# Performance work log

Measured on AMD Instinct MI355X. Metric: run time of the kernel, lower is better.

Reference implementation:

```python
import jax, jax.numpy as jnp
import numpy as np
import math

PERIODS = [4, 2, 1]          # period_num[-3:] sorted desc
SEQ, PRED, CH = 192, 96, 8
TOPM, DM = 20, 512
N_TRAIN, BSZ = 10000, 32


def decompose_mg(data):
    # data: [N, L, C] -> mg: [P, N, L, C], offset-removed (last step per period)
    N, L, C = data.shape
    mgs = []
    for g in PERIODS:
        cur = data.reshape(N, L // g, g, C).mean(axis=2)   # pooled
        cur = jnp.repeat(cur, g, axis=1)                   # repeat_interleave
        mgs.append(cur)
    mg = jnp.stack(mgs, axis=0)                            # [P, N, L, C]
    offset = mg[:, :, -1:, :]
    return mg - offset


def l2norm(x, eps=1e-12):
    n = jnp.sqrt(jnp.sum(x * x, axis=-1, keepdims=True))
    return x / jnp.maximum(n, eps)


def setup_inputs() -> dict:
    key = jax.random.key(0)
    ks = jax.random.split(key, 10)
    F = SEQ * CH
    return {
        "x": jax.random.normal(ks[0], (BSZ, SEQ, CH), dtype=jnp.float32),
        "index": jax.random.randint(ks[1], (BSZ,), 0, N_TRAIN),
        "train_data_all": jax.random.normal(ks[2], (N_TRAIN, SEQ, CH), dtype=jnp.float32),
        "y_data_all": jax.random.normal(ks[3], (N_TRAIN, PRED, CH), dtype=jnp.float32),
        "W_sim": jax.random.normal(ks[4], (F, F), dtype=jnp.float32) / math.sqrt(F),
        "b_sim": jax.random.normal(ks[5], (F,), dtype=jnp.float32) * 0.01,
        "Wq": jax.random.normal(ks[6], (CH, DM), dtype=jnp.float32) / math.sqrt(CH),
        "bq": jax.random.normal(ks[7], (DM,), dtype=jnp.float32) * 0.01,
        "Wk": jax.random.normal(ks[8], (CH, DM), dtype=jnp.float32) / math.sqrt(CH),
        "bk": jax.random.normal(ks[9], (DM,), dtype=jnp.float32) * 0.01,
    }


def reference(x, index, train_data_all, y_data_all, W_sim, b_sim, Wq, bq, Wk, bk):
    P = len(PERIODS)
    bsz = x.shape[0]
    n_train = train_data_all.shape[0]

    # multi-period decomposition (prepare_dataset + retrieve)
    train_mg = decompose_mg(train_data_all)   # [P, N, SEQ, CH]
    y_mg = decompose_mg(y_data_all)           # [P, N, PRED, CH]
    x_mg = decompose_mg(x)                    # [P, B, SEQ, CH]

    # periodic_batch_corr: shared linear then cosine similarity
    bx = x_mg.reshape(P, bsz, -1) @ W_sim + b_sim           # [P, B, F]
    ax = train_mg.reshape(P, n_train, -1) @ W_sim + b_sim   # [P, N, F]
    sim = jnp.einsum('pbf,pnf->pbn', l2norm(bx), l2norm(ax))

    # self-exclusion sliding mask (train=True)
    win = 2 * (SEQ + PRED) - 1
    slid = jnp.arange(win)[None, :] + (index - SEQ - PRED + 1)[:, None]
    slid = jnp.clip(slid, 0, n_train - 1)
    mask = jnp.zeros((bsz, n_train), dtype=bool).at[
        jnp.arange(bsz)[:, None], slid].set(True)
    sim = jnp.where(mask[None], -jnp.inf, sim)

    # top-m retrieval
    _, topm_idx = jax.lax.top_k(sim, TOPM)                  # [P, B, TOPM]

    # gather neighbors per period
    gather = jax.vmap(lambda src, i: src[i])                # over period axis
    k = gather(train_mg, topm_idx)                          # [P, B, M, SEQ, CH]
    v = gather(y_mg, topm_idx)                              # [P, B, M, PRED, CH]

    # cross attention (shared projections across periods)
    q_emb = x_mg @ Wq + bq                                  # [P, B, S, D]
    k_emb = k @ Wk + bk                                     # [P, B, M, T, D]
    scores = jnp.einsum('pbsd,pbmtd->pbsmt', q_emb, k_emb) / math.sqrt(DM)
    S = scores.shape[2]
    w = jax.nn.softmax(scores.reshape(P, bsz, S, TOPM * S), axis=-1)
    w = w.reshape(P, bsz, S, TOPM, S)
    nw = w.sum(axis=-1).sum(axis=2)                         # [P, B, M]
    nw = jax.nn.softmax(nw, axis=-1)
    out = jnp.einsum('pbm,pbmlc->pblc', nw, v)              # [P, B, PRED, CH]
    return out
```

## Files before the change

### kernel.cpp

```cpp
#include <hip/hip_runtime.h>
#include <hip/hip_bf16.h>
#include <math.h>

#define NPER 3
#define SEQL 192
#define PREDL 96
#define CH 8
#define FD 1536
#define NT 10000
#define BS 32
#define PB 96
#define TOPM 20
#define DM 512
#define HALFW 287
#define NROWS 30000
#define NRP2 10112
#define NRB2 79
#define NCB 12
#define PCOLS 24
#define NWG2 (NRB2*NCB)
#define NJ 3840
#define K0R 384
#define K1R 768
#define K2R 1536
#define KS 16
#define KSD 8
#define NCH 4
#define CHSZ (NT/NCH)
#define RSQRT_DM 0.04419417382415922f

typedef __attribute__((ext_vector_type(8))) short bf16x8;
typedef __attribute__((ext_vector_type(4))) float f32x4;
typedef __attribute__((address_space(3))) short lds_short_t;
typedef __attribute__((address_space(1))) const short glb_short_t;

__device__ inline float bflo(unsigned u){ return __uint_as_float(u << 16); }
__device__ inline float bfhi(unsigned u){ return __uint_as_float(u & 0xFFFF0000u); }
__device__ inline float bf2f(unsigned short u){ return __uint_as_float((unsigned)u << 16); }
__device__ inline unsigned short f2bf(float v){
  __hip_bfloat16 h = __float2bfloat16(v);
  return *reinterpret_cast<unsigned short*>(&h);
}

template<int L>
__global__ __launch_bounds__(256) void k_decompose(const float* __restrict__ data,
                                                   float* __restrict__ mg,
                                                   __hip_bfloat16* __restrict__ m0,
                                                   __hip_bfloat16* __restrict__ m1,
                                                   __hip_bfloat16* __restrict__ m2,
                                                   __hip_bfloat16* __restrict__ trH,
                                                   __hip_bfloat16* __restrict__ trL,
                                                   int N) {
  __shared__ float row[L*CH];
  __shared__ float m4[(L/4)*CH];
  __shared__ float m2s[(L/2)*CH];
  int n = blockIdx.x;
  const float* src = data + (size_t)n*L*CH;
  for (int e = threadIdx.x; e < L*CH/4; e += 256)
    *reinterpret_cast<float4*>(&row[e*4]) = *reinterpret_cast<const float4*>(&src[e*4]);
  __syncthreads();
  for (int i = threadIdx.x; i < (L/4)*CH; i += 256) {
    int j = i >> 3, c = i & 7;
    m4[i] = (row[(4*j)*CH+c] + row[(4*j+1)*CH+c] + row[(4*j+2)*CH+c] + row[(4*j+3)*CH+c]) * 0.25f;
  }
  for (int i = threadIdx.x; i < (L/2)*CH; i += 256) {
    int j = i >> 3, c = i & 7;
    m2s[i] = (row[(2*j)*CH+c] + row[(2*j+1)*CH+c]) * 0.5f;
  }
  __syncthreads();
  if (mg) {
    size_t plane = (size_t)N*L*CH;
    size_t base  = (size_t)n*L*CH;
    for (int e = threadIdx.x; e < L*CH/4; e += 256) {
      int i = e*4;
      int l = i >> 3, c0 = i & 7;
      float v0[4], v1[4], v2[4];
      #pragma unroll
      for (int j=0;j<4;j++) {
        int c = c0 + j;
        v0[j] = m4[(l>>2)*CH+c] - m4[(L/4-1)*CH+c];
        v1[j] = m2s[(l>>1)*CH+c] - m2s[(L/2-1)*CH+c];
        v2[j] = row[i+j] - row[(L-1)*CH+c];
      }
      *reinterpret_cast<float4*>(&mg[base+i])           = make_float4(v0[0],v0[1],v0[2],v0[3]);
      *reinterpret_cast<float4*>(&mg[plane+base+i])     = make_float4(v1[0],v1[1],v1[2],v1[3]);
      *reinterpret_cast<float4*>(&mg[2*plane+base+i])   = make_float4(v2[0],v2[1],v2[2],v2[3]);
    }
  }
  if (m0) {
    unsigned short* p0 = (unsigned short*)m0 + (size_t)n*K0R;
    unsigned short* p1 = (unsigned short*)m1 + (size_t)n*K1R;
    unsigned short* p2 = (unsigned short*)m2 + (size_t)n*K2R;
    for (int e = threadIdx.x; e < K0R/4; e += 256) {
      int i = e*4, c0 = i & 7;
      ushort4 u;
      u.x = f2bf(m4[i]   - m4[(L/4-1)*CH + c0]);
      u.y = f2bf(m4[i+1] - m4[(L/4-1)*CH + c0+1]);
      u.z = f2bf(m4[i+2] - m4[(L/4-1)*CH + c0+2]);
      u.w = f2bf(m4[i+3] - m4[(L/4-1)*CH + c0+3]);
      *reinterpret_cast<ushort4*>(&p0[i]) = u;
    }
    for (int e = threadIdx.x; e < K1R/4; e += 256) {
      int i = e*4, c0 = i & 7;
      ushort4 u;
      u.x = f2bf(m2s[i]   - m2s[(L/2-1)*CH + c0]);
      u.y = f2bf(m2s[i+1] - m2s[(L/2-1)*CH + c0+1]);
      u.z = f2bf(m2s[i+2] - m2s[(L/2-1)*CH + c0+2]);
      u.w = f2bf(m2s[i+3] - m2s[(L/2-1)*CH + c0+3]);
      *reinterpret_cast<ushort4*>(&p1[i]) = u;
    }
    for (int e = threadIdx.x; e < K2R/4; e += 256) {
      int i = e*4, c0 = i & 7;
      ushort4 u;
      u.x = f2bf(row[i]   - row[(L-1)*CH + c0]);
      u.y = f2bf(row[i+1] - row[(L-1)*CH + c0+1]);
      u.z = f2bf(row[i+2] - row[(L-1)*CH + c0+2]);
      u.w = f2bf(row[i+3] - row[(L-1)*CH + c0+3]);
      *reinterpret_cast<ushort4*>(&p2[i]) = u;
    }
  }
  if (trH) {
    unsigned short* h = (unsigned short*)trH + (size_t)n*L*CH;
    unsigned short* l = (unsigned short*)trL + (size_t)n*L*CH;
    for (int e = threadIdx.x; e < L*CH/4; e += 256) {
      int i = e*4;
      ushort4 uh, ul;
      uh.x = f2bf(row[i]);   ul.x = f2bf(row[i]   - bf2f(uh.x));
      uh.y = f2bf(row[i+1]); ul.y = f2bf(row[i+1] - bf2f(uh.y));
      uh.z = f2bf(row[i+2]); ul.z = f2bf(row[i+2] - bf2f(uh.z));
      uh.w = f2bf(row[i+3]); ul.w = f2bf(row[i+3] - bf2f(uh.w));
      *reinterpret_cast<ushort4*>(&h[i]) = uh;
      *reinterpret_cast<ushort4*>(&l[i]) = ul;
    }
  }
}

__global__ __launch_bounds__(256) void k_wtg_all(const float* __restrict__ W,
                                                 __hip_bfloat16* __restrict__ wt0,
                                                 __hip_bfloat16* __restrict__ wt1,
                                                 __hip_bfloat16* __restrict__ wt2,
                                                 const float* __restrict__ Wq,
                                                 const float* __restrict__ bq,
                                                 const float* __restrict__ Wk,
                                                 const float* __restrict__ bk,
                                                 float* __restrict__ cst) {
  __shared__ float t[128][33];
  int bx = blockIdx.x;
  if (bx == 84) {
    if (blockIdx.y != 0) return;
    int tt = threadIdx.x;
    if (tt < 64) {
      int c = tt >> 3, e = tt & 7;
      float s = 0.f;
      for (int d=0; d<DM; d++) s += Wq[c*DM+d] * Wk[e*DM+d];
      cst[tt] = s;
    } else if (tt < 72) {
      int c = tt - 64; float s=0.f;
      for (int d=0;d<DM;d++) s += Wq[c*DM+d]*bk[d];
      cst[tt] = s;
    } else if (tt < 80) {
      int e = tt - 72; float s=0.f;
      for (int d=0;d<DM;d++) s += Wk[e*DM+d]*bq[d];
      cst[tt] = s;
    } else if (tt == 80) {
      float s=0.f;
      for (int d=0;d<DM;d++) s += bq[d]*bk[d];
      cst[80] = s;
    }
    return;
  }
  int G, kr0, Kred;
  __hip_bfloat16* Wt;
  if (bx < 12)      { G = 4; kr0 = bx*32;      Kred = K0R; Wt = wt0; }
  else if (bx < 36) { G = 2; kr0 = (bx-12)*32; Kred = K1R; Wt = wt1; }
  else              { G = 1; kr0 = (bx-36)*32; Kred = K2R; Wt = wt2; }
  int f0 = blockIdx.y*32;
  int k0 = kr0*G;
  int tid = threadIdx.x, tx = tid & 31, ty = tid >> 5;
  for (int i = ty; i < 32*G; i += 8)
    t[i][tx] = W[(size_t)(k0+i)*FD + f0 + tx];
  __syncthreads();
  for (int fl = ty; fl < 32; fl += 8) {
    float s = 0.f;
    for (int i=0;i<G;i++) s += t[((tx>>3)*G+i)*8 + (tx&7)][fl];
    Wt[(size_t)(f0+fl)*Kred + kr0 + tx] = __float2bfloat16(s);
  }
}

__global__ __launch_bounds__(256) void k_bx_part(const float* __restrict__ xmg,
                                                 const float* __restrict__ W,
                                                 float* __restrict__ bxp) {
  __shared__ float xs[PB][17];
  __shared__ float Ws[16][65];
  int f0 = blockIdx.x * 64;
  int ks = blockIdx.y;
  int kbase = ks * (FD/KS);
  int tid = threadIdx.x;
  int fl = tid & 63, gp = tid >> 6;
  float acc[24];
  #pragma unroll
  for (int j=0;j<24;j++) acc[j]=0.f;
  for (int k0 = kbase; k0 < kbase + FD/KS; k0 += 16) {
    for (int e = tid; e < PB*16; e += 256) {
      int r = e >> 4, k = e & 15;
      xs[r][k] = xmg[(size_t)r*FD + k0 + k];
    }
    for (int e = tid; e < 16*64; e += 256) {
      int k = e >> 6, f = e & 63;
      Ws[k][f] = W[(size_t)(k0+k)*FD + f0 + f];
    }
    __syncthreads();
    #pragma unroll
    for (int kk = 0; kk < 16; kk++) {
      float w = Ws[kk][fl];
      #pragma unroll
      for (int j=0;j<24;j++) acc[j] += w * xs[gp + 4*j][kk];
    }
    __syncthreads();
  }
  #pragma unroll
  for (int j=0;j<24;j++) {
    int pb = gp + 4*j;
    bxp[((size_t)ks*PB + pb)*FD + f0 + fl] = acc[j];
  }
}

__global__ __launch_bounds__(256) void k_bxnorm(const float* __restrict__ bxp,
                                                const float* __restrict__ bsim,
                                                float* __restrict__ u_out,
                                                float* __restrict__ cpb) {
  __shared__ float rowv[FD];
  __shared__ float r1[256], r2[256];
  __shared__ float invs;
  int pb = blockIdx.x, tid = threadIdx.x;
  float s2 = 0.f, sb = 0.f;
  for (int f = tid; f < FD; f += 256) {
    float s = 0.f;
    #pragma unroll
    for (int ks=0; ks<KS; ks++) s += bxp[((size_t)ks*PB + pb)*FD + f];
    s += bsim[f];
    rowv[f] = s;
    s2 += s*s; sb += s*bsim[f];
  }
  r1[tid]=s2; r2[tid]=sb; __syncthreads();
  for (int off=128; off>0; off>>=1) {
    if (tid<off) { r1[tid]+=r1[tid+off]; r2[tid]+=r2[tid+off]; }
    __syncthreads();
  }
  if (tid==0) {
    float iv = 1.f / fmaxf(sqrtf(r1[0]), 1e-12f);
    invs = iv;
    cpb[pb] = r2[0] * iv;
  }
  __syncthreads();
  float iv = invs;
  for (int f = tid; f < FD; f += 256) u_out[(size_t)pb*FD + f] = rowv[f]*iv;
}

__global__ __launch_bounds__(256) void k_t_part(const float* __restrict__ u,
                                                const float* __restrict__ W,
                                                float* __restrict__ tp) {
  __shared__ float us[PB][17];
  __shared__ float Wt[64][17];
  int k0 = blockIdx.x * 64;
  int ks = blockIdx.y;
  int fbase = ks * (FD/KS);
  int tid = threadIdx.x;
  int kl = tid & 63, gp = tid >> 6;
  float acc[24];
  #pragma unroll
  for (int j=0;j<24;j++) acc[j]=0.f;
  for (int fc = fbase; fc < fbase + FD/KS; fc += 16) {
    for (int e = tid; e < PB*16; e += 256) {
      int r = e >> 4, f = e & 15;
      us[r][f] = u[(size_t)r*FD + fc + f];
    }
    for (int e = tid; e < 64*16; e += 256) {
      int k = e >> 4, f = e & 15;
      Wt[k][f] = W[(size_t)(k0+k)*FD + fc + f];
    }
    __syncthreads();
    #pragma unroll
    for (int ff = 0; ff < 16; ff++) {
      float w = Wt[kl][ff];
      #pragma unroll
      for (int j=0;j<24;j++) acc[j] += w * us[gp + 4*j][ff];
    }
    __syncthreads();
  }
  #pragma unroll
  for (int j=0;j<24;j++) {
    int pb = gp + 4*j;
    tp[((size_t)ks*PB + pb)*FD + k0 + kl] = acc[j];
  }
}

__global__ __launch_bounds__(192) void k_tred_adj(const float* __restrict__ tp,
                                                  __hip_bfloat16* __restrict__ tadjH,
                                                  __hip_bfloat16* __restrict__ tadjL) {
  __shared__ float ts[SEQL*CH];
  __shared__ float Tc[CH];
  int pb = blockIdx.x;
  int p = pb / BS;
  int g = (p==0) ? 4 : (p==1) ? 2 : 1;
  int l = threadIdx.x;
  #pragma unroll
  for (int c=0;c<CH;c++) {
    float s = 0.f;
    #pragma unroll
    for (int ks=0; ks<KS; ks++) s += tp[((size_t)ks*PB + pb)*FD + l*CH + c];
    ts[l*CH+c] = s;
  }
  __syncthreads();
  if (l < CH) {
    float s=0.f;
    for (int j=0;j<SEQL;j++) s += ts[j*CH+l];
    Tc[l] = s;
  }
  __syncthreads();
  int j0 = (l/g)*g;
  bool last = (j0 == SEQL-g);
  float ig = 1.f/(float)g;
  unsigned short* th = (unsigned short*)tadjH;
  unsigned short* tl = (unsigned short*)tadjL;
  #pragma unroll
  for (int c=0;c<CH;c++) {
    float s = 0.f;
    for (int jj=0;jj<g;jj++) s += ts[(j0+jj)*CH+c];
    float v = s*ig - (last ? Tc[c]*ig : 0.f);
    unsigned short hv = f2bf(v);
    th[(size_t)pb*FD + l*CH+c] = hv;
    tl[(size_t)pb*FD + l*CH+c] = f2bf(v - bf2f(hv));
  }
}

__global__ __launch_bounds__(256) void k_norm_mfma(
    const __hip_bfloat16* __restrict__ A0b, const __hip_bfloat16* __restrict__ A1b,
    const __hip_bfloat16* __restrict__ A2b,
    const __hip_bfloat16* __restrict__ B0b, const __hip_bfloat16* __restrict__ B1b,
    const __hip_bfloat16* __restrict__ B2b,
    const float* __restrict__ bsim, float* __restrict__ part) {
  __shared__ __align__(16) short lA[128*32];
  __shared__ __align__(16) short lB[128*32];
  int bid = blockIdx.x;
  int p, seg;
  if (bid < NWG2)        { p = 2; seg = bid; }
  else if (bid < 2*NWG2) { p = 1; seg = bid - NWG2; }
  else                   { p = 0; seg = bid - 2*NWG2; }
  const short* A = (const short*)(p==0 ? A0b : (p==1 ? A1b : A2b));
  const short* B = (const short*)(p==0 ? B0b : (p==1 ? B1b : B2b));
  int K = (p==0) ? K0R : ((p==1) ? K1R : K2R);
  int q = NWG2 >> 3, r = NWG2 & 7;
  int xcd = seg & 7, pos = seg >> 3;
  int wgid = (xcd < r ? xcd*(q+1) : r*(q+1) + (xcd-r)*q) + pos;
  int rb = wgid / NCB, cb = wgid - rb*NCB;
  int row0 = rb*128, col0 = cb*128;
  int tid = threadIdx.x, lane = tid & 63, wid = tid >> 6;
  int wr = (wid>>1)*64, wc = (wid&1)*64;

  size_t aoff[2], boff[2];
  int ldsb[2];
  #pragma unroll
  for (int i=0;i<2;i++) {
    int lrow = (wid*2+i)*16 + (lane>>2);
    int sl = lane & 3;
    int ss = (sl - lrow - (lrow>>2)) & 3;
    aoff[i] = (size_t)(row0 + lrow)*K + 8*ss;
    boff[i] = (size_t)(col0 + lrow)*K + 8*ss;
    ldsb[i] = (wid*2+i)*16*32;
  }

  f32x4 acc[4][4];
  #pragma unroll
  for (int m=0;m<4;m++)
    #pragma unroll
    for (int n=0;n<4;n++) acc[m][n] = (f32x4){0.f,0.f,0.f,0.f};

  int kslot = lane >> 4;
  for (int k0 = 0; k0 < K; k0 += 32) {
    #pragma unroll
    for (int i=0;i<2;i++) {
      __builtin_amdgcn_global_load_lds((glb_short_t*)(A + aoff[i] + k0),
                                       (lds_short_t*)&lA[ldsb[i]], 16, 0, 0);
      __builtin_amdgcn_global_load_lds((glb_short_t*)(B + boff[i] + k0),
                                       (lds_short_t*)&lB[ldsb[i]], 16, 0, 0);
    }
    __syncthreads();
    bf16x8 af[4], bfr[4];
    #pragma unroll
    for (int m=0;m<4;m++) {
      int rr = wr + m*16 + (lane&15);
      int s = (kslot + rr + (rr>>2)) & 3;
      af[m] = *(const bf16x8*)&lA[rr*32 + s*8];
    }
    #pragma unroll
    for (int n=0;n<4;n++) {
      int rr = wc + n*16 + (lane&15);
      int s = (kslot + rr + (rr>>2)) & 3;
      bfr[n] = *(const bf16x8*)&lB[rr*32 + s*8];
    }
    #pragma unroll
    for (int m=0;m<4;m++)
      #pragma unroll
      for (int n=0;n<4;n++)
        acc[m][n] = __builtin_amdgcn_mfma_f32_16x16x32_bf16(af[m], bfr[n], acc[m][n], 0, 0, 0);
    __syncthreads();
  }

  float bv[4];
  #pragma unroll
  for (int n=0;n<4;n++) bv[n] = bsim[col0 + wc + n*16 + (lane&15)];
  int pslot = cb*2 + (wid&1);
  #pragma unroll
  for (int m=0;m<4;m++) {
    #pragma unroll
    for (int j=0;j<4;j++) {
      float s = 0.f;
      #pragma unroll
      for (int n=0;n<4;n++) { float v = acc[m][n][j] + bv[n]; s += v*v; }
      s += __shfl_xor(s, 1); s += __shfl_xor(s, 2);
      s += __shfl_xor(s, 4); s += __shfl_xor(s, 8);
      if ((lane & 15) == 0) {
        int rr = row0 + wr + m*16 + (lane>>4)*4 + j;
        part[((size_t)p*NRP2 + rr)*PCOLS + pslot] = s;
      }
    }
  }
}

__global__ __launch_bounds__(256) void k_norm_red(const float* __restrict__ part,
                                                  float* __restrict__ norm2) {
  int r = blockIdx.x*256 + threadIdx.x;
  if (r < NROWS) {
    int p = r / NT, rr = r - p*NT;
    float s=0.f;
    #pragma unroll
    for (int cb=0; cb<PCOLS; cb++) s += part[((size_t)p*NRP2 + rr)*PCOLS + cb];
    norm2[r] = s;
  }
}

__global__ __launch_bounds__(256) void k_dot_mfma(
    const __hip_bfloat16* __restrict__ tadjHb, const __hip_bfloat16* __restrict__ tadjLb,
    const __hip_bfloat16* __restrict__ trHb, const __hip_bfloat16* __restrict__ trLb,
    float* __restrict__ dotp) {
  __shared__ __align__(16) short lAH[128*32];
  __shared__ __align__(16) short lAL[128*32];
  __shared__ __align__(16) short lBH[128*32];
  __shared__ __align__(16) short lBL[128*32];
  int bid = blockIdx.x;
  int ks = bid & 7, cbn = bid >> 3;
  int col0 = cbn * 128;
  int kbase = ks * (FD/KSD);
  int tid = threadIdx.x, lane = tid & 63, wid = tid >> 6;
  int wr = (wid>>1)*64, wc = (wid&1)*64;
  const short* AH = (const short*)tadjHb;
  const short* AL = (const short*)tadjLb;
  const short* BH = (const short*)trHb;
  const short* BL = (const short*)trLb;

  size_t aoff[2], boff[2];
  int ldsb[2];
  #pragma unroll
  for (int i=0;i<2;i++) {
    int lrow = (wid*2+i)*16 + (lane>>2);
    int sl = lane & 3;
    int ss = (sl - lrow - (lrow>>2)) & 3;
    aoff[i] = (size_t)lrow*FD + 8*ss;
    boff[i] = (size_t)(col0 + lrow)*FD + 8*ss;
    ldsb[i] = (wid*2+i)*16*32;
  }

  f32x4 acc[4][4];
  #pragma unroll
  for (int m=0;m<4;m++)
    #pragma unroll
    for (int n=0;n<4;n++) acc[m][n] = (f32x4){0.f,0.f,0.f,0.f};

  int kslot = lane >> 4;
  for (int k0 = kbase; k0 < kbase + FD/KSD; k0 += 32) {
    #pragma unroll
    for (int i=0;i<2;i++) {
      __builtin_amdgcn_global_load_lds((glb_short_t*)(AH + aoff[i] + k0),
                                       (lds_short_t*)&lAH[ldsb[i]], 16, 0, 0);
      __builtin_amdgcn_global_load_lds((glb_short_t*)(AL + aoff[i] + k0),
                                       (lds_short_t*)&lAL[ldsb[i]], 16, 0, 0);
      __builtin_amdgcn_global_load_lds((glb_short_t*)(BH + boff[i] + k0),
                                       (lds_short_t*)&lBH[ldsb[i]], 16, 0, 0);
      __builtin_amdgcn_global_load_lds((glb_short_t*)(BL + boff[i] + k0),
                                       (lds_short_t*)&lBL[ldsb[i]], 16, 0, 0);
    }
    __syncthreads();
    bf16x8 ah[4], al[4], bh[4], bl[4];
    #pragma unroll
    for (int m=0;m<4;m++) {
      int rr = wr + m*16 + (lane&15);
      int s = (kslot + rr + (rr>>2)) & 3;
      ah[m] = *(const bf16x8*)&lAH[rr*32 + s*8];
      al[m] = *(const bf16x8*)&lAL[rr*32 + s*8];
    }
    #pragma unroll
    for (int n=0;n<4;n++) {
      int rr = wc + n*16 + (lane&15);
      int s = (kslot + rr + (rr>>2)) & 3;
      bh[n] = *(const bf16x8*)&lBH[rr*32 + s*8];
      bl[n] = *(const bf16x8*)&lBL[rr*32 + s*8];
    }
    #pragma unroll
    for (int m=0;m<4;m++)
      #pragma unroll
      for (int n=0;n<4;n++) {
        acc[m][n] = __builtin_amdgcn_mfma_f32_16x16x32_bf16(ah[m], bh[n], acc[m][n], 0, 0, 0);
        acc[m][n] = __builtin_amdgcn_mfma_f32_16x16x32_bf16(ah[m], bl[n], acc[m][n], 0, 0, 0);
        acc[m][n] = __builtin_amdgcn_mfma_f32_16x16x32_bf16(al[m], bh[n], acc[m][n], 0, 0, 0);
      }
    __syncthreads();
  }

  #pragma unroll
  for (int m=0;m<4;m++) {
    int prow = wr + m*16 + (lane>>4)*4;
    if (prow >= PB) continue;
    #pragma unroll
    for (int n=0;n<4;n++) {
      int ncol = col0 + wc + n*16 + (lane&15);
      if (ncol >= NT) continue;
      #pragma unroll
      for (int j=0;j<4;j++) {
        dotp[((size_t)ks*PB + prow + j)*NT + ncol] = acc[m][n][j];
      }
    }
  }
}

__global__ __launch_bounds__(256) void k_topk_part(const float* __restrict__ dotp,
                                                   const float* __restrict__ cpb,
                                                   const float* __restrict__ norm2,
                                                   const int* __restrict__ index,
                                                   float* __restrict__ cv,
                                                   int* __restrict__ ci) {
  __shared__ float vals[CHSZ];
  __shared__ float rv[4];
  __shared__ int   ri[4];
  int pb = blockIdx.x, ch = blockIdx.y;
  int p = pb / BS, b = pb - p*BS;
  int n0 = ch*CHSZ;
  int tid = threadIdx.x, lane = tid & 63, wv = tid >> 6;
  int idx = index[b];
  int bl = idx - HALFW; if (bl < 0) bl = 0;
  int bh = idx + HALFW; if (bh > NT-1) bh = NT-1;
  const float* n2 = norm2 + (size_t)p*NT;
  float cp = cpb[pb];
  for (int i = tid; i < CHSZ; i += 256) {
    int n = n0 + i;
    float d = 0.f;
    #pragma unroll
    for (int ks=0; ks<KSD; ks++) d += dotp[((size_t)ks*PB + pb)*NT + n];
    d += cp;
    float v = d / fmaxf(sqrtf(n2[n]), 1e-12f);
    if (n >= bl && n <= bh) v = -INFINITY;
    vals[i] = v;
  }
  __syncthreads();
  for (int it = 0; it < TOPM; it++) {
    float bv = -INFINITY; int bi = CHSZ;
    for (int i = tid; i < CHSZ; i += 256) {
      float v = vals[i];
      if (v > bv) { bv = v; bi = i; }
    }
    #pragma unroll
    for (int off=32; off>0; off>>=1) {
      float ov = __shfl_xor(bv, off);
      int   oi = __shfl_xor(bi, off);
      if (ov > bv || (ov == bv && oi < bi)) { bv = ov; bi = oi; }
    }
    if (lane == 0) { rv[wv] = bv; ri[wv] = bi; }
    __syncthreads();
    if (tid == 0) {
      float fv = rv[0]; int fi = ri[0];
      #pragma unroll
      for (int w2=1; w2<4; w2++)
        if (rv[w2] > fv || (rv[w2] == fv && ri[w2] < fi)) { fv = rv[w2]; fi = ri[w2]; }
      cv[(pb*NCH + ch)*TOPM + it] = fv;
      ci[(pb*NCH + ch)*TOPM + it] = n0 + fi;
      vals[fi] = -INFINITY;
    }
    __syncthreads();
  }
}

__global__ __launch_bounds__(64) void k_topk_merge(const float* __restrict__ cv,
                                                   const int* __restrict__ ci,
                                                   int* __restrict__ topm) {
  __shared__ float v[NCH*TOPM];
  __shared__ int   id[NCH*TOPM];
  int pb = blockIdx.x;
  int lane = threadIdx.x;
  for (int i = lane; i < NCH*TOPM; i += 64) {
    v[i]  = cv[pb*NCH*TOPM + i];
    id[i] = ci[pb*NCH*TOPM + i];
  }
  __syncthreads();
  for (int it = 0; it < TOPM; it++) {
    float bv = -INFINITY; int bi = 0x7fffffff;
    for (int i = lane; i < NCH*TOPM; i += 64) {
      float vv = v[i];
      int ii = id[i];
      if (vv > bv || (vv == bv && ii < bi)) { bv = vv; bi = ii; }
    }
    #pragma unroll
    for (int off=32; off>0; off>>=1) {
      float ov = __shfl_xor(bv, off);
      int   oi = __shfl_xor(bi, off);
      if (ov > bv || (ov == bv && oi < bi)) { bv = ov; bi = oi; }
    }
    if (lane == 0) topm[pb*TOPM + it] = bi;
    for (int i = lane; i < NCH*TOPM; i += 64)
      if (id[i] == bi) v[i] = -INFINITY;
    __syncthreads();
  }
}

__global__ __launch_bounds__(256) void k_v(const float* __restrict__ ydata,
                                           const int* __restrict__ topm,
                                           float* __restrict__ vbuf) {
  __shared__ float row[PREDL*CH];
  __shared__ float m4[(PREDL/4)*CH];
  __shared__ float m2[(PREDL/2)*CH];
  int bm = blockIdx.x;
  int pb = bm / TOPM;
  int p = pb / BS;
  int n = topm[bm];
  int tid = threadIdx.x;
  const float* src = ydata + (size_t)n*PREDL*CH;
  for (int i=tid; i<PREDL*CH; i+=256) row[i]=src[i];
  __syncthreads();
  for (int i=tid; i<(PREDL/4)*CH; i+=256) {
    int j=i>>3, c=i&7;
    m4[i] = (row[(4*j)*CH+c]+row[(4*j+1)*CH+c]+row[(4*j+2)*CH+c]+row[(4*j+3)*CH+c])*0.25f;
  }
  for (int i=tid; i<(PREDL/2)*CH; i+=256) {
    int j=i>>3, c=i&7;
    m2[i] = (row[(2*j)*CH+c]+row[(2*j+1)*CH+c])*0.5f;
  }
  __syncthreads();
  float* dst = vbuf + (size_t)bm*PREDL*CH;
  for (int i=tid; i<PREDL*CH; i+=256) {
    int l=i>>3, c=i&7;
    float v;
    if (p==0)      v = m4[(l>>2)*CH+c] - m4[(PREDL/4-1)*CH+c];
    else if (p==1) v = m2[(l>>1)*CH+c] - m2[(PREDL/2-1)*CH+c];
    else           v = row[i] - row[(PREDL-1)*CH+c];
    dst[i] = v;
  }
}

template<int SH>
__device__ __forceinline__ void scores_body(
    const short* __restrict__ plane, int Kp,
    int pb, int sg,
    const int* __restrict__ topm,
    const float* __restrict__ xmg,
    const float* __restrict__ cst,
    float* __restrict__ nws,
    float* sc, int* tl, float* wred, float* lcst) {
  constexpr int UNQ = SEQL >> SH;
  constexpr int J   = TOPM * UNQ;
  constexpr int NU  = (J + 255) >> 8;
  constexpr bool FULL = (J % 256 == 0);
  int tid = threadIdx.x;
  int lane = tid & 63, wv = tid >> 6;
  if (tid < TOPM) tl[tid] = topm[pb*TOPM + tid];
  if (tid >= 32 && tid < 32+81) lcst[tid-32] = cst[tid-32];
  __syncthreads();
  uint4 kreg[NU];
  #pragma unroll
  for (int u=0; u<NU; u++) {
    int j = tid + u*256;
    if (FULL || j < J) {
      int m = j / UNQ, jj = j - m*UNQ;
      kreg[u] = *reinterpret_cast<const uint4*>(plane + (size_t)tl[m]*Kp + jj*8);
    }
  }
  for (int s8 = 0; s8 < 8; s8++) {
    int s = sg*8 + s8;
    int qr = pb*SEQL + s;
    float4 qa = *reinterpret_cast<const float4*>(&xmg[(size_t)qr*8]);
    float4 qc = *reinterpret_cast<const float4*>(&xmg[(size_t)qr*8+4]);
    float xq[8] = {qa.x,qa.y,qa.z,qa.w,qc.x,qc.y,qc.z,qc.w};
    float q[8];
    #pragma unroll
    for (int e=0;e<8;e++) {
      float ss = lcst[72+e];
      #pragma unroll
      for (int c=0;c<8;c++) ss += xq[c]*lcst[c*8+e];
      q[e] = ss;
    }
    float qb_s = lcst[80];
    #pragma unroll
    for (int c=0;c<8;c++) qb_s += xq[c]*lcst[64+c];
    float ms[NU];
    float lmax = -INFINITY;
    #pragma unroll
    for (int u=0; u<NU; u++) {
      int j = tid + u*256;
      if (FULL || j < J) {
        uint4 w = kreg[u];
        float s0 = qb_s;
        s0 += q[0]*bflo(w.x) + q[1]*bfhi(w.x);
        s0 += q[2]*bflo(w.y) + q[3]*bfhi(w.y);
        s0 += q[4]*bflo(w.z) + q[5]*bfhi(w.z);
        s0 += q[6]*bflo(w.w) + q[7]*bfhi(w.w);
        s0 *= RSQRT_DM;
        ms[u] = s0;
        lmax = fmaxf(lmax, s0);
      } else ms[u] = -INFINITY;
    }
    #pragma unroll
    for (int off=32; off>0; off>>=1) lmax = fmaxf(lmax, __shfl_xor(lmax, off));
    if (lane==0) wred[wv] = lmax;
    __syncthreads();
    float mx = fmaxf(fmaxf(wred[0],wred[1]),fmaxf(wred[2],wred[3]));
    float lsum = 0.f;
    #pragma unroll
    for (int u=0; u<NU; u++) {
      int j = tid + u*256;
      if (FULL || j < J) {
        float e = __expf(ms[u]-mx);
        sc[j] = e;
        lsum += e;
      }
    }
    #pragma unroll
    for (int off=32; off>0; off>>=1) lsum += __shfl_xor(lsum, off);
    if (lane==0) wred[4+wv] = lsum;
    __syncthreads();
    float invZ = 1.f / (wred[4]+wred[5]+wred[6]+wred[7]);
    for (int m = wv; m < TOPM; m += 4) {
      float v = 0.f;
      #pragma unroll
      for (int jj = 0; jj < UNQ; jj += 64) {
        int j2 = jj + lane;
        if (UNQ % 64 == 0 || j2 < UNQ) v += sc[m*UNQ + j2];
      }
      #pragma unroll
      for (int off=32; off>0; off>>=1) v += __shfl_xor(v, off);
      if (lane==0) nws[((size_t)pb*SEQL + s)*TOPM + m] = v * invZ;
    }
    __syncthreads();
  }
}

__global__ __launch_bounds__(256) void k_scores(const __hip_bfloat16* __restrict__ m0,
                                                const __hip_bfloat16* __restrict__ m1,
                                                const __hip_bfloat16* __restrict__ m2,
                                                const int* __restrict__ topm,
                                                const float* __restrict__ xmg,
                                                const float* __restrict__ cst,
                                                float* __restrict__ nws) {
  __shared__ float sc[NJ];
  __shared__ int tl[TOPM];
  __shared__ float wred[8];
  __shared__ float lcst[81];
  int pb = blockIdx.x, sg = blockIdx.y;
  int p = pb / BS;
  if (p == 0)
    scores_body<2>((const short*)m0, K0R, pb, sg, topm, xmg, cst, nws, sc, tl, wred, lcst);
  else if (p == 1)
    scores_body<1>((const short*)m1, K1R, pb, sg, topm, xmg, cst, nws, sc, tl, wred, lcst);
  else
    scores_body<0>((const short*)m2, K2R, pb, sg, topm, xmg, cst, nws, sc, tl, wred, lcst);
}

__global__ __launch_bounds__(256) void k_out(const float* __restrict__ nws,
                                             const float* __restrict__ vbuf,
                                             float* __restrict__ out) {
  __shared__ float nwp[TOPM];
  __shared__ float nwf[TOPM];
  int pb = blockIdx.x;
  int tid = threadIdx.x;
  if (tid < TOPM) {
    float s=0.f;
    for (int ss=0; ss<SEQL; ss++) s += nws[((size_t)pb*SEQL+ss)*TOPM + tid];
    nwp[tid] = s;
  }
  __syncthreads();
  if (tid==0) {
    float mx=-INFINITY;
    for (int m=0;m<TOPM;m++) mx=fmaxf(mx,nwp[m]);
    float Z=0.f;
    for (int m=0;m<TOPM;m++){ float e=expf(nwp[m]-mx); nwf[m]=e; Z+=e; }
    float iz=1.f/Z;
    for (int m=0;m<TOPM;m++) nwf[m]*=iz;
  }
  __syncthreads();
  for (int i=tid; i<PREDL*CH; i+=256) {
    float o=0.f;
    #pragma unroll
    for (int m=0;m<TOPM;m++) o += nwf[m]*vbuf[((size_t)pb*TOPM+m)*PREDL*CH + i];
    out[(size_t)pb*PREDL*CH + i] = o;
  }
}

extern "C" void kernel_launch(void* const* d_in, const int* in_sizes, int n_in,
                              void* d_out, int out_size, void* d_ws, size_t ws_size,
                              hipStream_t stream) {
  const float* x     = (const float*)d_in[0];
  const int*   index = (const int*)  d_in[1];
  const float* train = (const float*)d_in[2];
  const float* ydata = (const float*)d_in[3];
  const float* Wsim  = (const float*)d_in[4];
  const float* bsim  = (const float*)d_in[5];
  const float* Wq    = (const float*)d_in[6];
  const float* bq    = (const float*)d_in[7];
  const float* Wk    = (const float*)d_in[8];
  const float* bk    = (const float*)d_in[9];
  float* out = (float*)d_out;

  float* ws = (float*)d_ws;
  size_t off = 0;
  auto alloc = [&](size_t n)->float* { float* pp = ws + off; off += (n + 63) & ~(size_t)63; return pp; };
  __hip_bfloat16* m0b = (__hip_bfloat16*)alloc((size_t)NRP2*K0R/2);
  __hip_bfloat16* m1b = (__hip_bfloat16*)alloc((size_t)NRP2*K1R/2);
  __hip_bfloat16* m2b = (__hip_bfloat16*)alloc((size_t)NRP2*K2R/2);
  __hip_bfloat16* wt0 = (__hip_bfloat16*)alloc((size_t)FD*K0R/2);
  __hip_bfloat16* wt1 = (__hip_bfloat16*)alloc((size_t)FD*K1R/2);
  __hip_bfloat16* wt2 = (__hip_bfloat16*)alloc((size_t)FD*K2R/2);
  __hip_bfloat16* trH = (__hip_bfloat16*)alloc((size_t)NRP2*FD/2);
  __hip_bfloat16* trL = (__hip_bfloat16*)alloc((size_t)NRP2*FD/2);
  __hip_bfloat16* tadjH = (__hip_bfloat16*)alloc((size_t)128*FD/2);
  __hip_bfloat16* tadjL = (__hip_bfloat16*)alloc((size_t)128*FD/2);
  float* x_mg     = alloc((size_t)NPER*BS*FD);
  float* bx       = alloc((size_t)PB*FD);
  float* cpb      = alloc(PB);
  float* gpart    = alloc((size_t)KS*PB*FD);
  float* part     = alloc((size_t)NPER*NRP2*PCOLS);
  float* norm2    = alloc(NROWS);
  float* dotp     = alloc((size_t)KSD*PB*NT);
  float* cv       = alloc((size_t)PB*NCH*TOPM);
  int*   ci       = (int*)alloc(PB*NCH*TOPM);
  int*   topm     = (int*)alloc(PB*TOPM);
  float* cst      = alloc(128);
  float* vbuf     = alloc((size_t)PB*TOPM*PREDL*CH);
  float* nws      = alloc((size_t)PB*SEQL*TOPM);
  if (off * sizeof(float) > ws_size) return;

  k_decompose<SEQL><<<BS, 256, 0, stream>>>(x, x_mg, nullptr, nullptr, nullptr,
                                            nullptr, nullptr, BS);
  k_decompose<SEQL><<<NT, 256, 0, stream>>>(train, nullptr, m0b, m1b, m2b,
                                            trH, trL, NT);
  k_wtg_all<<<dim3(85, 48), 256, 0, stream>>>(Wsim, wt0, wt1, wt2, Wq, bq, Wk, bk, cst);
  k_bx_part<<<dim3(24, KS), 256, 0, stream>>>(x_mg, Wsim, gpart);
  k_bxnorm<<<PB, 256, 0, stream>>>(gpart, bsim, bx, cpb);
  k_t_part<<<dim3(24, KS), 256, 0, stream>>>(bx, Wsim, gpart);
  k_tred_adj<<<PB, 192, 0, stream>>>(gpart, tadjH, tadjL);
  k_norm_mfma<<<3*NWG2, 256, 0, stream>>>(m0b, m1b, m2b, wt0, wt1, wt2, bsim, part);
  k_norm_red<<<(NROWS+255)/256, 256, 0, stream>>>(part, norm2);
  k_dot_mfma<<<NRB2*KSD, 256, 0, stream>>>(tadjH, tadjL, trH, trL, dotp);
  k_topk_part<<<dim3(PB, NCH), 256, 0, stream>>>(dotp, cpb, norm2, index, cv, ci);
  k_topk_merge<<<PB, 64, 0, stream>>>(cv, ci, topm);
  k_v<<<PB*TOPM, 256, 0, stream>>>(ydata, topm, vbuf);
  k_scores<<<dim3(PB, 24), 256, 0, stream>>>(m0b, m1b, m2b, topm, x_mg, cst, nws);
  k_out<<<PB, 256, 0, stream>>>(nws, vbuf, out);
}
```

Measured before the change: 436.9 us.

## Merge independent kernels into combined launches to cut launch gaps

```diff
diff --git a/kernel.cpp b/kernel.cpp
--- a/kernel.cpp
+++ b/kernel.cpp
@@ -27,6 +27,8 @@
 #define KSD 8
 #define NCH 4
 #define CHSZ (NT/NCH)
+#define NWTG 4080
+#define NB_DOT (NRB2*KSD)
 #define RSQRT_DM 0.04419417382415922f
 
 typedef __attribute__((ext_vector_type(8))) short bf16x8;
@@ -43,18 +45,17 @@
 }
 
 template<int L>
-__global__ __launch_bounds__(256) void k_decompose(const float* __restrict__ data,
-                                                   float* __restrict__ mg,
-                                                   __hip_bfloat16* __restrict__ m0,
-                                                   __hip_bfloat16* __restrict__ m1,
-                                                   __hip_bfloat16* __restrict__ m2,
-                                                   __hip_bfloat16* __restrict__ trH,
-                                                   __hip_bfloat16* __restrict__ trL,
-                                                   int N) {
-  __shared__ float row[L*CH];
-  __shared__ float m4[(L/4)*CH];
-  __shared__ float m2s[(L/2)*CH];
-  int n = blockIdx.x;
+__device__ __forceinline__ void dec_body(const float* __restrict__ data,
+                                         float* __restrict__ mg,
+                                         __hip_bfloat16* __restrict__ m0,
+                                         __hip_bfloat16* __restrict__ m1,
+                                         __hip_bfloat16* __restrict__ m2,
+                                         __hip_bfloat16* __restrict__ trH,
+                                         __hip_bfloat16* __restrict__ trL,
+                                         int N, int n, float* fpool) {
+  float* row = fpool;
+  float* m4  = fpool + L*CH;
+  float* m2s = fpool + L*CH + (L/4)*CH;
   const float* src = data + (size_t)n*L*CH;
   for (int e = threadIdx.x; e < L*CH/4; e += 256)
     *reinterpret_cast<float4*>(&row[e*4]) = *reinterpret_cast<const float4*>(&src[e*4]);
@@ -135,19 +136,19 @@
   }
 }
 
-__global__ __launch_bounds__(256) void k_wtg_all(const float* __restrict__ W,
-                                                 __hip_bfloat16* __restrict__ wt0,
-                                                 __hip_bfloat16* __restrict__ wt1,
-                                                 __hip_bfloat16* __restrict__ wt2,
-                                                 const float* __restrict__ Wq,
-                                                 const float* __restrict__ bq,
-                                                 const float* __restrict__ Wk,
-                                                 const float* __restrict__ bk,
-                                                 float* __restrict__ cst) {
-  __shared__ float t[128][33];
-  int bx = blockIdx.x;
-  if (bx == 84) {
-    if (blockIdx.y != 0) return;
+__device__ __forceinline__ void wtg_body(const float* __restrict__ W,
+                                         __hip_bfloat16* __restrict__ wt0,
+                                         __hip_bfloat16* __restrict__ wt1,
+                                         __hip_bfloat16* __restrict__ wt2,
+                                         const float* __restrict__ Wq,
+                                         const float* __restrict__ bq,
+                                         const float* __restrict__ Wk,
+                                         const float* __restrict__ bk,
+                                         float* __restrict__ cst,
+                                         int wb, float* fpool) {
+  int bxx = wb / 48, byy = wb % 48;
+  if (bxx == 84) {
+    if (byy != 0) return;
     int tt = threadIdx.x;
     if (tt < 64) {
       int c = tt >> 3, e = tt & 7;
@@ -171,19 +172,48 @@
   }
   int G, kr0, Kred;
   __hip_bfloat16* Wt;
-  if (bx < 12)      { G = 4; kr0 = bx*32;      Kred = K0R; Wt = wt0; }
-  else if (bx < 36) { G = 2; kr0 = (bx-12)*32; Kred = K1R; Wt = wt1; }
-  else              { G = 1; kr0 = (bx-36)*32; Kred = K2R; Wt = wt2; }
-  int f0 = blockIdx.y*32;
+  if (bxx < 12)      { G = 4; kr0 = bxx*32;      Kred = K0R; Wt = wt0; }
+  else if (bxx < 36) { G = 2; kr0 = (bxx-12)*32; Kred = K1R; Wt = wt1; }
+  else               { G = 1; kr0 = (bxx-36)*32; Kred = K2R; Wt = wt2; }
+  int f0 = byy*32;
   int k0 = kr0*G;
   int tid = threadIdx.x, tx = tid & 31, ty = tid >> 5;
   for (int i = ty; i < 32*G; i += 8)
-    t[i][tx] = W[(size_t)(k0+i)*FD + f0 + tx];
+    fpool[i*33 + tx] = W[(size_t)(k0+i)*FD + f0 + tx];
   __syncthreads();
   for (int fl = ty; fl < 32; fl += 8) {
     float s = 0.f;
-    for (int i=0;i<G;i++) s += t[((tx>>3)*G+i)*8 + (tx&7)][fl];
+    for (int i=0;i<G;i++) s += fpool[(((tx>>3)*G+i)*8 + (tx&7))*33 + fl];
     Wt[(size_t)(f0+fl)*Kred + kr0 + tx] = __float2bfloat16(s);
+  }
+}
+
+__global__ __launch_bounds__(256) void k_front(const float* __restrict__ x,
+                                               const float* __restrict__ train,
+                                               float* __restrict__ x_mg,
+                                               __hip_bfloat16* __restrict__ m0,
+                                               __hip_bfloat16* __restrict__ m1,
+                                               __hip_bfloat16* __restrict__ m2,
+                                               __hip_bfloat16* __restrict__ trH,
+                                               __hip_bfloat16* __restrict__ trL,
+                                               const float* __restrict__ W,
+                                               __hip_bfloat16* __restrict__ wt0,
+                                               __hip_bfloat16* __restrict__ wt1,
+                                               __hip_bfloat16* __restrict__ wt2,
+                                               const float* __restrict__ Wq,
+                                               const float* __restrict__ bq,
+                                               const float* __restrict__ Wk,
+                                               const float* __restrict__ bk,
+                                               float* __restrict__ cst) {
+  __shared__ float fpool[128*33];
+  int bid = blockIdx.x;
+  if (bid < NT) {
+    dec_body<SEQL>(train, nullptr, m0, m1, m2, trH, trL, NT, bid, fpool);
+  } else if (bid < NT + NWTG) {
+    wtg_body(W, wt0, wt1, wt2, Wq, bq, Wk, bk, cst, bid - NT, fpool);
+  } else {
+    dec_body<SEQL>(x, x_mg, nullptr, nullptr, nullptr, nullptr, nullptr,
+                   BS, bid - NT - NWTG, fpool);
   }
 }
 
@@ -334,22 +364,14 @@
   }
 }
 
-__global__ __launch_bounds__(256) void k_norm_mfma(
-    const __hip_bfloat16* __restrict__ A0b, const __hip_bfloat16* __restrict__ A1b,
-    const __hip_bfloat16* __restrict__ A2b,
-    const __hip_bfloat16* __restrict__ B0b, const __hip_bfloat16* __restrict__ B1b,
-    const __hip_bfloat16* __restrict__ B2b,
-    const float* __restrict__ bsim, float* __restrict__ part) {
-  __shared__ __align__(16) short lA[128*32];
-  __shared__ __align__(16) short lB[128*32];
-  int bid = blockIdx.x;
-  int p, seg;
-  if (bid < NWG2)        { p = 2; seg = bid; }
-  else if (bid < 2*NWG2) { p = 1; seg = bid - NWG2; }
-  else                   { p = 0; seg = bid - 2*NWG2; }
-  const short* A = (const short*)(p==0 ? A0b : (p==1 ? A1b : A2b));
-  const short* B = (const short*)(p==0 ? B0b : (p==1 ? B1b : B2b));
-  int K = (p==0) ? K0R : ((p==1) ? K1R : K2R);
+__device__ __forceinline__ void norm_body(const short* __restrict__ A,
+                                          const short* __restrict__ B,
+                                          int K, int p, int seg,
+                                          const float* __restrict__ bsim,
+                                          float* __restrict__ part,
+                                          short* pool) {
+  short* lA = pool;
+  short* lB = pool + 128*32;
   int q = NWG2 >> 3, r = NWG2 & 7;
   int xcd = seg & 7, pos = seg >> 3;
   int wgid = (xcd < r ? xcd*(q+1) : r*(q+1) + (xcd-r)*q) + pos;
@@ -428,36 +450,21 @@
   }
 }
 
-__global__ __launch_bounds__(256) void k_norm_red(const float* __restrict__ part,
-                                                  float* __restrict__ norm2) {
-  int r = blockIdx.x*256 + threadIdx.x;
-  if (r < NROWS) {
-    int p = r / NT, rr = r - p*NT;
-    float s=0.f;
-    #pragma unroll
-    for (int cb=0; cb<PCOLS; cb++) s += part[((size_t)p*NRP2 + rr)*PCOLS + cb];
-    norm2[r] = s;
-  }
-}
-
-__global__ __launch_bounds__(256) void k_dot_mfma(
-    const __hip_bfloat16* __restrict__ tadjHb, const __hip_bfloat16* __restrict__ tadjLb,
-    const __hip_bfloat16* __restrict__ trHb, const __hip_bfloat16* __restrict__ trLb,
-    float* __restrict__ dotp) {
-  __shared__ __align__(16) short lAH[128*32];
-  __shared__ __align__(16) short lAL[128*32];
-  __shared__ __align__(16) short lBH[128*32];
-  __shared__ __align__(16) short lBL[128*32];
-  int bid = blockIdx.x;
-  int ks = bid & 7, cbn = bid >> 3;
+__device__ __forceinline__ void dot_body(const short* __restrict__ AH,
+                                         const short* __restrict__ AL,
+                                         const short* __restrict__ BH,
+                                         const short* __restrict__ BL,
+                                         float* __restrict__ dotp,
+                                         int dbid, short* pool) {
+  short* lAH = pool;
+  short* lAL = pool + 128*32;
+  short* lBH = pool + 2*128*32;
+  short* lBL = pool + 3*128*32;
+  int ks = dbid & 7, cbn = dbid >> 3;
   int col0 = cbn * 128;
   int kbase = ks * (FD/KSD);
   int tid = threadIdx.x, lane = tid & 63, wid = tid >> 6;
   int wr = (wid>>1)*64, wc = (wid&1)*64;
-  const short* AH = (const short*)tadjHb;
-  const short* AL = (const short*)tadjLb;
-  const short* BH = (const short*)trHb;
-  const short* BL = (const short*)trLb;
 
   size_t aoff[2], boff[2];
   int ldsb[2];
@@ -530,6 +537,42 @@
         dotp[((size_t)ks*PB + prow + j)*NT + ncol] = acc[m][n][j];
       }
     }
+  }
+}
+
+__global__ __launch_bounds__(256) void k_gemms(
+    const __hip_bfloat16* __restrict__ A0b, const __hip_bfloat16* __restrict__ A1b,
+    const __hip_bfloat16* __restrict__ A2b,
+    const __hip_bfloat16* __restrict__ B0b, const __hip_bfloat16* __restrict__ B1b,
+    const __hip_bfloat16* __restrict__ B2b,
+    const float* __restrict__ bsim, float* __restrict__ part,
+    const __hip_bfloat16* __restrict__ tadjHb, const __hip_bfloat16* __restrict__ tadjLb,
+    const __hip_bfloat16* __restrict__ trHb, const __hip_bfloat16* __restrict__ trLb,
+    float* __restrict__ dotp) {
+  __shared__ __align__(16) short pool[4*128*32];
+  int bid = blockIdx.x;
+  if (bid < NWG2) {
+    norm_body((const short*)A2b, (const short*)B2b, K2R, 2, bid, bsim, part, pool);
+  } else if (bid < 2*NWG2) {
+    norm_body((const short*)A1b, (const short*)B1b, K1R, 1, bid - NWG2, bsim, part, pool);
+  } else if (bid < 2*NWG2 + NB_DOT) {
+    dot_body((const short*)tadjHb, (const short*)tadjLb,
+             (const short*)trHb, (const short*)trLb, dotp, bid - 2*NWG2, pool);
+  } else {
+    norm_body((const short*)A0b, (const short*)B0b, K0R, 0,
+              bid - 2*NWG2 - NB_DOT, bsim, part, pool);
+  }
+}
+
+__global__ __launch_bounds__(256) void k_norm_red(const float* __restrict__ part,
+                                                  float* __restrict__ norm2) {
+  int r = blockIdx.x*256 + threadIdx.x;
+  if (r < NROWS) {
+    int p = r / NT, rr = r - p*NT;
+    float s=0.f;
+    #pragma unroll
+    for (int cb=0; cb<PCOLS; cb++) s += part[((size_t)p*NRP2 + rr)*PCOLS + cb];
+    norm2[r] = s;
   }
 }
 
@@ -621,13 +664,13 @@
   }
 }
 
-__global__ __launch_bounds__(256) void k_v(const float* __restrict__ ydata,
-                                           const int* __restrict__ topm,
-                                           float* __restrict__ vbuf) {
-  __shared__ float row[PREDL*CH];
-  __shared__ float m4[(PREDL/4)*CH];
-  __shared__ float m2[(PREDL/2)*CH];
-  int bm = blockIdx.x;
+__device__ __forceinline__ void v_body(const float* __restrict__ ydata,
+                                       const int* __restrict__ topm,
+                                       float* __restrict__ vbuf,
+                                       int bm, float* bpool) {
+  float* row = bpool;
+  float* m4  = bpool + 768;
+  float* m2  = bpool + 960;
   int pb = bm / TOPM;
   int p = pb / BS;
   int n = topm[bm];
@@ -751,25 +794,33 @@
   }
 }
 
-__global__ __launch_bounds__(256) void k_scores(const __hip_bfloat16* __restrict__ m0,
-                                                const __hip_bfloat16* __restrict__ m1,
-                                                const __hip_bfloat16* __restrict__ m2,
-                                                const int* __restrict__ topm,
-                                                const float* __restrict__ xmg,
-                                                const float* __restrict__ cst,
-                                                float* __restrict__ nws) {
-  __shared__ float sc[NJ];
-  __shared__ int tl[TOPM];
-  __shared__ float wred[8];
-  __shared__ float lcst[81];
-  int pb = blockIdx.x, sg = blockIdx.y;
-  int p = pb / BS;
-  if (p == 0)
-    scores_body<2>((const short*)m0, K0R, pb, sg, topm, xmg, cst, nws, sc, tl, wred, lcst);
-  else if (p == 1)
-    scores_body<1>((const short*)m1, K1R, pb, sg, topm, xmg, cst, nws, sc, tl, wred, lcst);
-  else
-    scores_body<0>((const short*)m2, K2R, pb, sg, topm, xmg, cst, nws, sc, tl, wred, lcst);
+__global__ __launch_bounds__(256) void k_back(const __hip_bfloat16* __restrict__ m0,
+                                              const __hip_bfloat16* __restrict__ m1,
+                                              const __hip_bfloat16* __restrict__ m2,
+                                              const int* __restrict__ topm,
+                                              const float* __restrict__ xmg,
+                                              const float* __restrict__ cst,
+                                              float* __restrict__ nws,
+                                              const float* __restrict__ ydata,
+                                              float* __restrict__ vbuf) {
+  __shared__ float bpool[3968];
+  int bid = blockIdx.x;
+  if (bid < PB*24) {
+    int pb = bid / 24, sg = bid - (bid/24)*24;
+    int p = pb / BS;
+    float* sc = bpool;
+    int* tl = (int*)(bpool + 3840);
+    float* wred = bpool + 3864;
+    float* lcst = bpool + 3872;
+    if (p == 0)
+      scores_body<2>((const short*)m0, K0R, pb, sg, topm, xmg, cst, nws, sc, tl, wred, lcst);
+    else if (p == 1)
+      scores_body<1>((const short*)m1, K1R, pb, sg, topm, xmg, cst, nws, sc, tl, wred, lcst);
+    else
+      scores_body<0>((const short*)m2, K2R, pb, sg, topm, xmg, cst, nws, sc, tl, wred, lcst);
+  } else {
+    v_body(ydata, topm, vbuf, bid - PB*24, bpool);
+  }
 }
 
 __global__ __launch_bounds__(256) void k_out(const float* __restrict__ nws,
@@ -845,21 +896,18 @@
   float* nws      = alloc((size_t)PB*SEQL*TOPM);
   if (off * sizeof(float) > ws_size) return;
 
-  k_decompose<SEQL><<<BS, 256, 0, stream>>>(x, x_mg, nullptr, nullptr, nullptr,
-                                            nullptr, nullptr, BS);
-  k_decompose<SEQL><<<NT, 256, 0, stream>>>(train, nullptr, m0b, m1b, m2b,
-                                            trH, trL, NT);
-  k_wtg_all<<<dim3(85, 48), 256, 0, stream>>>(Wsim, wt0, wt1, wt2, Wq, bq, Wk, bk, cst);
+  k_front<<<NT + NWTG + BS, 256, 0, stream>>>(x, train, x_mg, m0b, m1b, m2b, trH, trL,
+                                              Wsim, wt0, wt1, wt2, Wq, bq, Wk, bk, cst);
   k_bx_part<<<dim3(24, KS), 256, 0, stream>>>(x_mg, Wsim, gpart);
   k_bxnorm<<<PB, 256, 0, stream>>>(gpart, bsim, bx, cpb);
   k_t_part<<<dim3(24, KS), 256, 0, stream>>>(bx, Wsim, gpart);
   k_tred_adj<<<PB, 192, 0, stream>>>(gpart, tadjH, tadjL);
-  k_norm_mfma<<<3*NWG2, 256, 0, stream>>>(m0b, m1b, m2b, wt0, wt1, wt2, bsim, part);
+  k_gemms<<<3*NWG2 + NB_DOT, 256, 0, stream>>>(m0b, m1b, m2b, wt0, wt1, wt2, bsim, part,
+                                               tadjH, tadjL, trH, trL, dotp);
   k_norm_red<<<(NROWS+255)/256, 256, 0, stream>>>(part, norm2);
-  k_dot_mfma<<<NRB2*KSD, 256, 0, stream>>>(tadjH, tadjL, trH, trL, dotp);
   k_topk_part<<<dim3(PB, NCH), 256, 0, stream>>>(dotp, cpb, norm2, index, cv, ci);
   k_topk_merge<<<PB, 64, 0, stream>>>(cv, ci, topm);
-  k_v<<<PB*TOPM, 256, 0, stream>>>(ydata, topm, vbuf);
-  k_scores<<<dim3(PB, 24), 256, 0, stream>>>(m0b, m1b, m2b, topm, x_mg, cst, nws);
+  k_back<<<PB*24 + PB*TOPM, 256, 0, stream>>>(m0b, m1b, m2b, topm, x_mg, cst, nws,
+                                              ydata, vbuf);
   k_out<<<PB, 256, 0, stream>>>(nws, vbuf, out);
 }
```

Result: faster. 425.0 us (-2.7%).
